# Kernel optimization log

Measured on AMD Instinct MI355X. Metric: run time of the kernel, lower is better.

## Reference

```python
import jax, jax.numpy as jnp
import numpy as np

B, L, S, H, E = 4, 2048, 2048, 8, 64

def setup_inputs() -> dict:
    key = jax.random.key(0)
    kq, kk, kv, kt, kd = jax.random.split(key, 5)
    return {
        "queries": jax.random.normal(kq, (B, L, H, E), dtype=jnp.float32),
        "keys": jax.random.normal(kk, (B, S, H, E), dtype=jnp.float32),
        "values": jax.random.normal(kv, (B, S, H, E), dtype=jnp.float32),
        "attn_mask": jnp.zeros((1,), dtype=bool),
        "tau": jax.random.uniform(kt, (B, 1), dtype=jnp.float32),
        "delta": jax.random.normal(kd, (B, 1), dtype=jnp.float32),
    }

def reference(queries, keys, values, attn_mask, tau, delta):
    # queries: [B,L,H,E], keys: [B,S,H,E], values: [B,S,H,D]
    Bq, Lq, Hq, Eq = queries.shape
    scale = 1.0 / jnp.sqrt(jnp.float32(Eq))
    scores = jnp.einsum('blhe,bshe->bhls', queries, keys)  # [B,H,L,S]
    scores = scores * tau.reshape(Bq, 1, 1, 1)             # per-batch tau scale
    scores = scores + delta.reshape(Bq, 1, 1, 1)           # per-batch delta bias
    A = jax.nn.softmax(scale * scores, axis=-1)            # dropout is identity at eval
    V = jnp.einsum('bhls,bshd->blhd', A, values)           # [B,L,H,D]
    return V
```

## Files before the change

### kernel.cpp

```cpp
#include <hip/hip_runtime.h>
#include <hip/hip_bf16.h>
#include <stdint.h>

#define LL 2048
#define SS 2048
#define HH 8
#define EE 64
#define RSG 512

typedef float v4f  __attribute__((ext_vector_type(4)));
typedef float v16f __attribute__((ext_vector_type(16)));
typedef short s4v  __attribute__((ext_vector_type(4)));
typedef short s8v  __attribute__((ext_vector_type(8)));

__device__ __forceinline__ short f2bf(float f) {
    unsigned u = __float_as_uint(f);
    u = (u + 0x7fffu + ((u >> 16) & 1u)) >> 16;
    return (short)u;
}

__device__ __forceinline__ s4v pack4bf(float a, float b, float c, float d) {
    float2 ab = make_float2(a, b), cd = make_float2(c, d);
    __hip_bfloat162 r0 = __float22bfloat162_rn(ab);
    __hip_bfloat162 r1 = __float22bfloat162_rn(cd);
    s4v r;
    __builtin_memcpy(&r, &r0, 4);
    __builtin_memcpy(((char*)&r) + 4, &r1, 4);
    return r;
}

__global__ __launch_bounds__(256)
void dsattn_prep(const float* __restrict__ kk, const float* __restrict__ vv,
                 short* __restrict__ kbf, short* __restrict__ vimg)
{
    __shared__ float T[64][68];
    const int t = threadIdx.x;
    const int blk = blockIdx.x;
    if (blk < 1024) {
        const float* src = kk + (size_t)blk * 4096;
        short* dst = kbf + (size_t)blk * 4096;
        #pragma unroll
        for (int c = 0; c < 4; ++c) {
            v4f d = *(const v4f*)(src + (c * 256 + t) * 4);
            *(s4v*)(dst + (c * 256 + t) * 4) = pack4bf(d[0], d[1], d[2], d[3]);
        }
    } else {
        const int vb = blk - 1024;
        const int b = vb >> 8, h = (vb >> 5) & 7, ts = vb & 31;
        const float* vp = vv + ((size_t)b * SS + ts * 64) * RSG + h * EE;
        #pragma unroll
        for (int c = 0; c < 4; ++c) {
            int idx = c * 256 + t, s = idx >> 4, e0 = (idx & 15) << 2;
            *(v4f*)&T[s][e0] = *(const v4f*)(vp + (size_t)s * RSG + e0);
        }
        __syncthreads();
        short* dst = vimg + (size_t)vb * 4096;
        #pragma unroll
        for (int half = 0; half < 2; ++half) {
            int ci = half * 256 + t;
            int e = ci >> 3, pos = ci & 7;
            int c = pos ^ (e & 7);
            int sbase = 16 * (c >> 1) + 4 * (c & 1);
            s8v ov;
            #pragma unroll
            for (int j = 0; j < 8; ++j) {
                int s = sbase + 8 * (j >> 2) + (j & 3);
                ov[j] = f2bf(T[s][e]);
            }
            *(s8v*)(dst + ci * 8) = ov;
        }
    }
}

__global__ __launch_bounds__(256, 2)
void dsattn_main(const float* __restrict__ q, const short* __restrict__ kbf,
                 const short* __restrict__ vimg, const float* __restrict__ tau,
                 float* __restrict__ out)
{
    __shared__ short KV[2][8192];

    const int t    = threadIdx.x;
    const int lane = t & 63;
    const int w    = t >> 6;
    const int l31  = lane & 31;
    const int hi   = lane >> 5;
    const int mt = blockIdx.x, h = blockIdx.y, b = blockIdx.z;

    const float scf = 0.125f * 1.44269504088896f * tau[b];

    s8v qf[4];
    {
        const float* qb = q + ((size_t)b * LL + (size_t)mt * 128 + w * 32 + l31) * RSG
                            + h * EE + 8 * hi;
        #pragma unroll
        for (int ks = 0; ks < 4; ++ks) {
            v4f a0 = *(const v4f*)(qb + 16 * ks);
            v4f a1 = *(const v4f*)(qb + 16 * ks + 4);
            s4v p0 = pack4bf(a0[0] * scf, a0[1] * scf, a0[2] * scf, a0[3] * scf);
            s4v p1 = pack4bf(a1[0] * scf, a1[1] * scf, a1[2] * scf, a1[3] * scf);
            s8v f;
            #pragma unroll
            for (int j = 0; j < 4; ++j) { f[j] = p0[j]; f[4 + j] = p1[j]; }
            qf[ks] = f;
        }
    }

    const char* gsrc;
    int jstr, tstr;
    if (w < 2) {
        int i = w * 256 + lane;
        int row = i >> 3;
        int c = (i & 7) ^ (row & 7);
        gsrc = (const char*)(kbf + (size_t)b * (SS * RSG) + h * EE) + row * (RSG * 2) + c * 16;
        jstr = 8 * RSG * 2;
        tstr = 64 * RSG * 2;
    } else {
        int i2 = (w - 2) * 256 + lane;
        gsrc = (const char*)(vimg + (((size_t)b * HH + h) * 32) * 4096) + i2 * 16;
        jstr = 1024; tstr = 8192;
    }

    #define STAGE(p)                                                                      \
        {                                                                                 \
            _Pragma("unroll")                                                             \
            for (int j = 0; j < 4; ++j) {                                                 \
                __builtin_amdgcn_global_load_lds(                                         \
                    (const __attribute__((address_space(1))) unsigned*)(gsrc + j * jstr), \
                    (__attribute__((address_space(3))) unsigned*)&KV[p][w * 2048 + j * 512], \
                    16, 0, 0);                                                            \
            }                                                                             \
            gsrc += tstr;                                                                 \
        }

    v16f oacc[2];
    #pragma unroll
    for (int mb = 0; mb < 2; ++mb)
        #pragma unroll
        for (int r = 0; r < 16; ++r) oacc[mb][r] = 0.0f;
    float rsum = 0.0f;

    const int xo = l31 & 7;
    const int rbase = l31 * 64;
    int kpos[4];
    #pragma unroll
    for (int ks = 0; ks < 4; ++ks) kpos[ks] = (((hi + 2 * ks) & 7) ^ xo) * 8;

    STAGE(0);

    for (int it = 0; it < 32; ++it) {
        const int p = it & 1;
        __syncthreads();
        if (it < 31) STAGE(p ^ 1);

        const short* Kp = &KV[p][0];
        const short* Vp = &KV[p][4096];

        v16f st[2];
        #pragma unroll
        for (int mb = 0; mb < 2; ++mb) {
            v16f z;
            #pragma unroll
            for (int r = 0; r < 16; ++r) z[r] = 0.0f;
            #pragma unroll
            for (int ks = 0; ks < 4; ++ks) {
                s8v kf = *(const s8v*)&Kp[mb * 2048 + rbase + kpos[ks]];
                z = __builtin_amdgcn_mfma_f32_32x32x16_bf16(kf, qf[ks], z, 0, 0, 0);
            }
            st[mb] = z;
        }

        #pragma unroll
        for (int mb = 0; mb < 2; ++mb)
            #pragma unroll
            for (int r = 0; r < 16; ++r)
                st[mb][r] = __builtin_amdgcn_exp2f(st[mb][r]);
        float s0 = 0.f, s1 = 0.f;
        #pragma unroll
        for (int r = 0; r < 16; ++r) { s0 += st[0][r]; s1 += st[1][r]; }
        rsum += s0 + s1;

        s8v pf[4];
        #pragma unroll
        for (int tt = 0; tt < 4; ++tt) {
            int o = 8 * (tt & 1);
            const v16f& sv = st[tt >> 1];
            s4v lo = pack4bf(sv[o + 0], sv[o + 1], sv[o + 2], sv[o + 3]);
            s4v hs = pack4bf(sv[o + 4], sv[o + 5], sv[o + 6], sv[o + 7]);
            s8v f;
            #pragma unroll
            for (int j = 0; j < 4; ++j) { f[j] = lo[j]; f[4 + j] = hs[j]; }
            pf[tt] = f;
        }

        #pragma unroll
        for (int mb = 0; mb < 2; ++mb) {
            v16f acc = oacc[mb];
            #pragma unroll
            for (int ks = 0; ks < 4; ++ks) {
                s8v vf = *(const s8v*)&Vp[mb * 2048 + rbase + kpos[ks]];
                acc = __builtin_amdgcn_mfma_f32_32x32x16_bf16(vf, pf[ks], acc, 0, 0, 0);
            }
            oacc[mb] = acc;
        }
    }

    rsum += __shfl_xor(rsum, 32);
    const float inv = 1.0f / rsum;
    float* ob = out + ((size_t)b * LL + (size_t)mt * 128 + w * 32 + l31) * RSG + h * EE;
    #pragma unroll
    for (int mb = 0; mb < 2; ++mb)
        #pragma unroll
        for (int rq = 0; rq < 4; ++rq) {
            int e0 = 32 * mb + 8 * rq + 4 * hi;
            v4f o4 = { oacc[mb][4 * rq + 0] * inv, oacc[mb][4 * rq + 1] * inv,
                       oacc[mb][4 * rq + 2] * inv, oacc[mb][4 * rq + 3] * inv };
            *(v4f*)(ob + e0) = o4;
        }
}

extern "C" void kernel_launch(void* const* d_in, const int* in_sizes, int n_in,
                              void* d_out, int out_size, void* d_ws, size_t ws_size,
                              hipStream_t stream) {
    const float* q     = (const float*)d_in[0];
    const float* k     = (const float*)d_in[1];
    const float* v     = (const float*)d_in[2];
    const float* tau   = (const float*)d_in[4];
    float* out = (float*)d_out;

    short* kbf  = (short*)d_ws;
    short* vimg = kbf + (size_t)4 * SS * RSG;

    dsattn_prep<<<dim3(2048), dim3(256), 0, stream>>>(k, v, kbf, vimg);
    dsattn_main<<<dim3(LL / 128, HH, 4), dim3(256), 0, stream>>>(q, kbf, vimg, tau, out);
}
```

Baseline: 135.9 us.

## Deepen LDS ring to four stages and overlap QK with previous PV

Grows the shared K/V staging ring from two to four buffers and issues loads two tiles ahead. The loop is software-pipelined so each iteration runs the QK^T MFMAs for tile it and the PV MFMAs for tile it-1, letting exp and pack work interleave with matrix ops. `__syncthreads` is replaced by an explicit `s_waitcnt vmcnt(4)` plus `s_barrier`, so only the oldest staged tile has to land before the barrier. This hides more global-to-LDS latency but doubles LDS per block to 64KB and keeps more registers live, which may limit occupancy.

```diff
diff --git a/kernel.cpp b/kernel.cpp
--- a/kernel.cpp
+++ b/kernel.cpp
@@ -77,7 +77,7 @@
                  const short* __restrict__ vimg, const float* __restrict__ tau,
                  float* __restrict__ out)
 {
-    __shared__ short KV[2][8192];
+    __shared__ short KV[4][8192];
 
     const int t    = threadIdx.x;
     const int lane = t & 63;
@@ -145,64 +145,103 @@
     #pragma unroll
     for (int ks = 0; ks < 4; ++ks) kpos[ks] = (((hi + 2 * ks) & 7) ^ xo) * 8;
 
+    s8v pf[4];
+
+    #define DO_QK(tt, st)                                                          \
+        {                                                                          \
+            const short* Kp = &KV[(tt) & 3][0];                                    \
+            _Pragma("unroll")                                                      \
+            for (int mb = 0; mb < 2; ++mb) {                                       \
+                v16f z;                                                            \
+                _Pragma("unroll")                                                  \
+                for (int r = 0; r < 16; ++r) z[r] = 0.0f;                          \
+                _Pragma("unroll")                                                  \
+                for (int ks = 0; ks < 4; ++ks) {                                   \
+                    s8v kf = *(const s8v*)&Kp[mb * 2048 + rbase + kpos[ks]];       \
+                    z = __builtin_amdgcn_mfma_f32_32x32x16_bf16(kf, qf[ks], z, 0, 0, 0); \
+                }                                                                  \
+                st[mb] = z;                                                        \
+            }                                                                      \
+        }
+
+    #define DO_PV(tt)                                                              \
+        {                                                                          \
+            const short* Vp = &KV[(tt) & 3][4096];                                 \
+            _Pragma("unroll")                                                      \
+            for (int mb = 0; mb < 2; ++mb) {                                       \
+                v16f acc = oacc[mb];                                               \
+                _Pragma("unroll")                                                  \
+                for (int ks = 0; ks < 4; ++ks) {                                   \
+                    s8v vf = *(const s8v*)&Vp[mb * 2048 + rbase + kpos[ks]];       \
+                    acc = __builtin_amdgcn_mfma_f32_32x32x16_bf16(vf, pf[ks], acc, 0, 0, 0); \
+                }                                                                  \
+                oacc[mb] = acc;                                                    \
+            }                                                                      \
+        }
+
+    #define DO_EXP(st)                                                             \
+        {                                                                          \
+            _Pragma("unroll")                                                      \
+            for (int mb = 0; mb < 2; ++mb)                                         \
+                _Pragma("unroll")                                                  \
+                for (int r = 0; r < 16; ++r)                                       \
+                    st[mb][r] = __builtin_amdgcn_exp2f(st[mb][r]);                 \
+            float s0 = 0.f, s1 = 0.f;                                              \
+            _Pragma("unroll")                                                      \
+            for (int r = 0; r < 16; ++r) { s0 += st[0][r]; s1 += st[1][r]; }       \
+            rsum += s0 + s1;                                                       \
+            _Pragma("unroll")                                                      \
+            for (int tt2 = 0; tt2 < 4; ++tt2) {                                    \
+                int o = 8 * (tt2 & 1);                                             \
+                const v16f& sv = st[tt2 >> 1];                                     \
+                s4v lo = pack4bf(sv[o + 0], sv[o + 1], sv[o + 2], sv[o + 3]);      \
+                s4v hs = pack4bf(sv[o + 4], sv[o + 5], sv[o + 6], sv[o + 7]);      \
+                s8v f;                                                             \
+                _Pragma("unroll")                                                  \
+                for (int j = 0; j < 4; ++j) { f[j] = lo[j]; f[4 + j] = hs[j]; }    \
+                pf[tt2] = f;                                                       \
+            }                                                                      \
+        }
+
+    #define WAITBAR(n)                                                             \
+        asm volatile("s_waitcnt vmcnt(" #n ") lgkmcnt(0)" ::: "memory");           \
+        asm volatile("s_barrier" ::: "memory");
+
     STAGE(0);
-
-    for (int it = 0; it < 32; ++it) {
-        const int p = it & 1;
-        __syncthreads();
-        if (it < 31) STAGE(p ^ 1);
-
-        const short* Kp = &KV[p][0];
-        const short* Vp = &KV[p][4096];
-
-        v16f st[2];
-        #pragma unroll
-        for (int mb = 0; mb < 2; ++mb) {
-            v16f z;
-            #pragma unroll
-            for (int r = 0; r < 16; ++r) z[r] = 0.0f;
-            #pragma unroll
-            for (int ks = 0; ks < 4; ++ks) {
-                s8v kf = *(const s8v*)&Kp[mb * 2048 + rbase + kpos[ks]];
-                z = __builtin_amdgcn_mfma_f32_32x32x16_bf16(kf, qf[ks], z, 0, 0, 0);
-            }
-            st[mb] = z;
-        }
-
-        #pragma unroll
-        for (int mb = 0; mb < 2; ++mb)
-            #pragma unroll
-            for (int r = 0; r < 16; ++r)
-                st[mb][r] = __builtin_amdgcn_exp2f(st[mb][r]);
-        float s0 = 0.f, s1 = 0.f;
-        #pragma unroll
-        for (int r = 0; r < 16; ++r) { s0 += st[0][r]; s1 += st[1][r]; }
-        rsum += s0 + s1;
-
-        s8v pf[4];
-        #pragma unroll
-        for (int tt = 0; tt < 4; ++tt) {
-            int o = 8 * (tt & 1);
-            const v16f& sv = st[tt >> 1];
-            s4v lo = pack4bf(sv[o + 0], sv[o + 1], sv[o + 2], sv[o + 3]);
-            s4v hs = pack4bf(sv[o + 4], sv[o + 5], sv[o + 6], sv[o + 7]);
-            s8v f;
-            #pragma unroll
-            for (int j = 0; j < 4; ++j) { f[j] = lo[j]; f[4 + j] = hs[j]; }
-            pf[tt] = f;
-        }
-
-        #pragma unroll
-        for (int mb = 0; mb < 2; ++mb) {
-            v16f acc = oacc[mb];
-            #pragma unroll
-            for (int ks = 0; ks < 4; ++ks) {
-                s8v vf = *(const s8v*)&Vp[mb * 2048 + rbase + kpos[ks]];
-                acc = __builtin_amdgcn_mfma_f32_32x32x16_bf16(vf, pf[ks], acc, 0, 0, 0);
-            }
-            oacc[mb] = acc;
-        }
-    }
+    STAGE(1);
+
+    {
+        WAITBAR(4);
+        STAGE(2);
+        v16f st[2];
+        DO_QK(0, st);
+        DO_EXP(st);
+    }
+
+    for (int it = 1; it < 30; ++it) {
+        WAITBAR(4);
+        STAGE((it + 2) & 3);
+        v16f st[2];
+        DO_QK(it, st);
+        DO_PV(it - 1);
+        DO_EXP(st);
+    }
+
+    {
+        WAITBAR(4);
+        v16f st[2];
+        DO_QK(30, st);
+        DO_PV(29);
+        DO_EXP(st);
+    }
+    {
+        WAITBAR(0);
+        v16f st[2];
+        DO_QK(31, st);
+        DO_PV(30);
+        DO_EXP(st);
+    }
+    DO_PV(31);
 
     rsum += __shfl_xor(rsum, 32);
     const float inv = 1.0f / rsum;
@@ -221,10 +260,10 @@
 extern "C" void kernel_launch(void* const* d_in, const int* in_sizes, int n_in,
                               void* d_out, int out_size, void* d_ws, size_t ws_size,
                               hipStream_t stream) {
-    const float* q     = (const float*)d_in[0];
-    const float* k     = (const float*)d_in[1];
-    const float* v     = (const float*)d_in[2];
-    const float* tau   = (const float*)d_in[4];
+    const float* q   = (const float*)d_in[0];
+    const float* k   = (const float*)d_in[1];
+    const float* v   = (const float*)d_in[2];
+    const float* tau = (const float*)d_in[4];
     float* out = (float*)d_out;
 
     short* kbf  = (short*)d_ws;
```

Result: slower. 138.9 us (+2.2%).
